# Performance work log

Hardware: AMD Instinct MI355X
Metric: run time of the kernel (lower is better)

Reference implementation:

```python
import jax, jax.numpy as jnp
import numpy as np
from jax import lax

N, DEG, D_IN, D_FEAT, D_HID, D_REP, G = 32768, 16, 128, 256, 256, 128, 64


def setup_inputs() -> dict:
    key = jax.random.key(0)
    ks = jax.random.split(key, 24)
    def w(k, shape):
        return (jax.random.normal(k, shape, jnp.float32) / np.sqrt(shape[0])).astype(jnp.float32)
    inp = {
        "in_feat": jax.random.normal(ks[0], (N, D_IN), jnp.float32),
        "neighbors": jax.random.randint(ks[1], (N, DEG), 0, N, jnp.int32),
        "node2graph": jnp.sort(jax.random.randint(ks[2], (N,), 0, G, jnp.int32)),
        # layer 1 (SAGEConv 128 -> 256, lstm aggregator: LSTM(128,128))
        "w_ih1": w(ks[3], (4 * D_IN, D_IN)),
        "w_hh1": w(ks[4], (4 * D_IN, D_IN)),
        "b_lstm1": jnp.zeros((4 * D_IN,), jnp.float32),
        "w_self1": w(ks[5], (D_IN, D_FEAT)),
        "w_neigh1": w(ks[6], (D_IN, D_FEAT)),
        "b1": jnp.zeros((D_FEAT,), jnp.float32),
        # layer 2 (SAGEConv 256 -> 256, LSTM(256,256))
        "w_ih2": w(ks[7], (4 * D_FEAT, D_FEAT)),
        "w_hh2": w(ks[8], (4 * D_FEAT, D_FEAT)),
        "b_lstm2": jnp.zeros((4 * D_FEAT,), jnp.float32),
        "w_self2": w(ks[9], (D_FEAT, D_HID)),
        "w_neigh2": w(ks[10], (D_FEAT, D_HID)),
        "b2": jnp.zeros((D_HID,), jnp.float32),
        # heads
        "w_mu": w(ks[11], (D_HID, D_REP)),
        "b_mu": jnp.zeros((D_REP,), jnp.float32),
        "w_sigma": w(ks[12], (D_HID, D_REP)),
        "b_sigma": jnp.zeros((D_REP,), jnp.float32),
    }
    return inp


def _lstm_agg(seq, w_ih, w_hh, b):
    # seq: [N, L, D] neighbor messages; LSTM with zero init, return final hidden h.
    n, _, d = seq.shape
    h0 = jnp.zeros((n, d), seq.dtype)
    def step(carry, x):
        h, c = carry
        gates = x @ w_ih.T + h @ w_hh.T + b  # [N, 4D]
        i, f, g, o = jnp.split(gates, 4, axis=-1)  # pytorch gate order i,f,g,o
        c = jax.nn.sigmoid(f) * c + jax.nn.sigmoid(i) * jnp.tanh(g)
        h = jax.nn.sigmoid(o) * jnp.tanh(c)
        return (h, c), None
    (h, _), _ = lax.scan(step, (h0, h0), jnp.swapaxes(seq, 0, 1))
    return h


def _sage_lstm(feat, neighbors, w_ih, w_hh, b_lstm, w_self, w_neigh, b):
    msgs = feat[neighbors]                      # irregular gather [N, DEG, D]
    h_n = _lstm_agg(msgs, w_ih, w_hh, b_lstm)   # [N, D]
    return feat @ w_self + h_n @ w_neigh + b


def reference(in_feat, neighbors, node2graph,
              w_ih1, w_hh1, b_lstm1, w_self1, w_neigh1, b1,
              w_ih2, w_hh2, b_lstm2, w_self2, w_neigh2, b2,
              w_mu, b_mu, w_sigma, b_sigma):
    h = _sage_lstm(in_feat, neighbors, w_ih1, w_hh1, b_lstm1, w_self1, w_neigh1, b1)
    h = jax.nn.relu(h)
    h = _sage_lstm(h, neighbors, w_ih2, w_hh2, b_lstm2, w_self2, w_neigh2, b2)
    # dgl.mean_nodes: per-graph mean over nodes
    sums = jax.ops.segment_sum(h, node2graph, num_segments=G)
    cnts = jax.ops.segment_sum(jnp.ones((h.shape[0],), h.dtype), node2graph, num_segments=G)
    x = sums / jnp.maximum(cnts, 1.0)[:, None]
    return (x @ w_mu + b_mu, x @ w_sigma + b_sigma)
```

## Files before the change

### kernel.cpp

```cpp
#include <hip/hip_runtime.h>
#include <hip/hip_bf16.h>
#include <cstddef>

#define NN_   32768
#define DEG_  16
#define D1_   128
#define D2_   256
#define G_    64
#define DREP_ 128

typedef __attribute__((ext_vector_type(8))) short bf16x8;
typedef __attribute__((ext_vector_type(4))) float f32x4;
typedef __attribute__((ext_vector_type(4))) unsigned short us4;
typedef unsigned short ushort_t;

__device__ __attribute__((aligned(16))) ushort_t g_feat1[(size_t)NN_ * D1_];
__device__ __attribute__((aligned(16))) ushort_t g_hfeat[(size_t)NN_ * D2_];
__device__ __attribute__((aligned(16))) ushort_t g_hA[(size_t)NN_ * D2_];
__device__ __attribute__((aligned(16))) ushort_t g_hB[(size_t)NN_ * D2_];
__device__ __attribute__((aligned(16))) ushort_t g_c[(size_t)NN_ * D2_];
__device__ __attribute__((aligned(16))) ushort_t g_P[(size_t)NN_ * 1024];
__device__ __attribute__((aligned(16))) float    g_outh[(size_t)NN_ * D2_];
__device__ __attribute__((aligned(16))) ushort_t g_wih1[512 * 128];
__device__ __attribute__((aligned(16))) ushort_t g_whh1[512 * 128];
__device__ __attribute__((aligned(16))) ushort_t g_wself1[256 * 128];
__device__ __attribute__((aligned(16))) ushort_t g_wneigh1[256 * 128];
__device__ __attribute__((aligned(16))) ushort_t g_wih2[1024 * 256];
__device__ __attribute__((aligned(16))) ushort_t g_whh2[1024 * 256];
__device__ __attribute__((aligned(16))) ushort_t g_wself2[256 * 256];
__device__ __attribute__((aligned(16))) ushort_t g_wneigh2[256 * 256];
__device__ float g_gsum[G_ * D2_];
__device__ int   g_gcnt[G_];

__device__ __forceinline__ ushort_t f2bf(float f) {
    unsigned int u = __float_as_uint(f);
    u += 0x7fffu + ((u >> 16) & 1u);
    return (ushort_t)(u >> 16);
}
__device__ __forceinline__ float bf2f(ushort_t u) {
    return __uint_as_float(((unsigned int)u) << 16);
}
__device__ __forceinline__ float sigf(float x) { return 1.f / (1.f + __expf(-x)); }
__device__ __forceinline__ float tanhf_(float x) { return 1.f - 2.f / (__expf(2.f * x) + 1.f); }

__global__ __launch_bounds__(256) void cvt_bf16(const float* __restrict__ src,
                                                ushort_t* __restrict__ dst, int n)
{
    int i = blockIdx.x * 256 + threadIdx.x;
    if (i < n) dst[i] = f2bf(src[i]);
}

__global__ __launch_bounds__(256) void cvt_bf16_T(const float* __restrict__ src,
                                                  ushort_t* __restrict__ dst, int K, int N)
{
    int i = blockIdx.x * 256 + threadIdx.x;
    if (i < K * N) {
        int k = i / N, n = i % N;
        dst[n * K + k] = f2bf(src[i]);
    }
}

template<bool DUAL, bool HAS_BIAS, bool RELU, bool OUTBF>
__global__ __launch_bounds__(256) void gemm_mfma(
    const ushort_t* __restrict__ A1, const ushort_t* __restrict__ B1,
    const ushort_t* __restrict__ A2, const ushort_t* __restrict__ B2,
    const float* __restrict__ bias, float* __restrict__ Cf,
    ushort_t* __restrict__ Cb, int M, int N, int K)
{
    __shared__ ushort_t As[64][72];
    __shared__ ushort_t Bs[64][72];
    const int tid = threadIdx.x;
    const int l = tid & 63, w = tid >> 6;
    const int m0 = blockIdx.y * 64, n0 = blockIdx.x * 64;

    f32x4 acc[4];
#pragma unroll
    for (int m = 0; m < 4; ++m) acc[m] = (f32x4){0.f, 0.f, 0.f, 0.f};

    const int npass = DUAL ? 2 : 1;
    for (int pass = 0; pass < npass; ++pass) {
        const ushort_t* __restrict__ A = (DUAL && pass) ? A2 : A1;
        const ushort_t* __restrict__ B = (DUAL && pass) ? B2 : B1;
        for (int k0 = 0; k0 < K; k0 += 64) {
#pragma unroll
            for (int i = 0; i < 2; ++i) {
                int cid = tid + 256 * i;
                int row = cid >> 3, col = (cid & 7) * 8;
                *(uint4*)&As[row][col] = *(const uint4*)&A[(size_t)(m0 + row) * K + k0 + col];
                *(uint4*)&Bs[row][col] = *(const uint4*)&B[(size_t)(n0 + row) * K + k0 + col];
            }
            __syncthreads();
#pragma unroll
            for (int kk = 0; kk < 64; kk += 32) {
                bf16x8 b = *(const bf16x8*)&Bs[16 * w + (l & 15)][kk + (l >> 4) * 8];
#pragma unroll
                for (int m = 0; m < 4; ++m) {
                    bf16x8 a = *(const bf16x8*)&As[16 * m + (l & 15)][kk + (l >> 4) * 8];
                    acc[m] = __builtin_amdgcn_mfma_f32_16x16x32_bf16(a, b, acc[m], 0, 0, 0);
                }
            }
            __syncthreads();
        }
    }

#pragma unroll
    for (int m = 0; m < 4; ++m) {
#pragma unroll
        for (int r = 0; r < 4; ++r) {
            int row = m0 + 16 * m + (l >> 4) * 4 + r;
            int col = n0 + 16 * w + (l & 15);
            float v = acc[m][r];
            if (HAS_BIAS) v += bias[col];
            if (RELU) v = fmaxf(v, 0.f);
            if (OUTBF) Cb[(size_t)row * N + col] = f2bf(v);
            else       Cf[(size_t)row * N + col] = v;
        }
    }
}

template<int D>
__global__ __launch_bounds__(256, 3) void lstm_step5(
    const ushort_t* __restrict__ h_prev, const ushort_t* __restrict__ whh,
    const ushort_t* __restrict__ P, const int* __restrict__ nbr,
    ushort_t* __restrict__ c, ushort_t* __restrict__ h_next, int t)
{
    constexpr int HP = D + 8;
    constexpr int KC = D / 32;
    constexpr int NT = 4;
    constexpr int NU = D / 64;
    __shared__ ushort_t As[64][HP];

    const int tid = threadIdx.x;
    const int l = tid & 63, w = tid >> 6;
    const int lr = l & 15, lg = l >> 4;
    const int m0 = blockIdx.x * 64;

    int js[NT];
#pragma unroll
    for (int nt = 0; nt < NT; ++nt)
        js[nt] = nbr[(size_t)(m0 + nt * 16 + lr) * DEG_ + t];

    constexpr int CH = 64 * D / 8;
#pragma unroll
    for (int cid = tid; cid < CH; cid += 256) {
        int row = cid / (D / 8), cc = (cid % (D / 8)) * 8;
        *(uint4*)&As[row][cc] = *(const uint4*)&h_prev[(size_t)(m0 + row) * D + cc];
    }
    __syncthreads();

#pragma unroll
    for (int u = 0; u < NU; ++u) {
        const int d0 = u * 64;
        const int dd = d0 + w * 16 + lg * 4;

        us4 pg[NT][4];
#pragma unroll
        for (int nt = 0; nt < NT; ++nt) {
            const size_t base = (size_t)js[nt] * (4 * D) + dd;
#pragma unroll
            for (int g = 0; g < 4; ++g)
                pg[nt][g] = *(const us4*)&P[base + g * D];
        }

        f32x4 acc[4][NT];
#pragma unroll
        for (int g = 0; g < 4; ++g)
#pragma unroll
            for (int nt = 0; nt < NT; ++nt) acc[g][nt] = (f32x4){0.f, 0.f, 0.f, 0.f};

        const ushort_t* __restrict__ wbase =
            &whh[(size_t)(d0 + w * 16 + lr) * D + lg * 8];
#pragma unroll
        for (int kc = 0; kc < KC; ++kc) {
            bf16x8 a[4];
#pragma unroll
            for (int g = 0; g < 4; ++g)
                a[g] = *(const bf16x8*)&wbase[(size_t)g * D * D + kc * 32];
#pragma unroll
            for (int nt = 0; nt < NT; ++nt) {
                bf16x8 b = *(const bf16x8*)&As[nt * 16 + lr][kc * 32 + lg * 8];
#pragma unroll
                for (int g = 0; g < 4; ++g)
                    acc[g][nt] = __builtin_amdgcn_mfma_f32_16x16x32_bf16(
                        a[g], b, acc[g][nt], 0, 0, 0);
            }
        }

#pragma unroll
        for (int nt = 0; nt < NT; ++nt) {
            const size_t ci = (size_t)(m0 + nt * 16 + lr) * D + dd;
            us4 cold = *(const us4*)&c[ci];
            us4 cnew, hnew;
#pragma unroll
            for (int r = 0; r < 4; ++r) {
                float gi = acc[0][nt][r] + bf2f(pg[nt][0][r]);
                float gf = acc[1][nt][r] + bf2f(pg[nt][1][r]);
                float gg = acc[2][nt][r] + bf2f(pg[nt][2][r]);
                float go = acc[3][nt][r] + bf2f(pg[nt][3][r]);
                float cn = sigf(gf) * bf2f(cold[r]) + sigf(gi) * tanhf_(gg);
                cnew[r] = f2bf(cn);
                hnew[r] = f2bf(sigf(go) * tanhf_(cn));
            }
            *(us4*)&c[ci] = cnew;
            *(us4*)&h_next[ci] = hnew;
        }
    }
}

template<int D>
__global__ __launch_bounds__(256) void cell_first(
    const ushort_t* __restrict__ P, const int* __restrict__ nbr,
    ushort_t* __restrict__ c, ushort_t* __restrict__ h_out)
{
    int idx = blockIdx.x * 256 + threadIdx.x;
    int n = idx / D, d = idx % D;
    int j = nbr[n * DEG_];
    size_t base = (size_t)j * (4 * D);
    float gi = bf2f(P[base + d]);
    float gg = bf2f(P[base + 2 * D + d]);
    float go = bf2f(P[base + 3 * D + d]);
    float cn = sigf(gi) * tanhf_(gg);
    c[idx] = f2bf(cn);
    h_out[idx] = f2bf(sigf(go) * tanhf_(cn));
}

__global__ void graph_counts(const int* __restrict__ n2g, int* __restrict__ cnt)
{
    __shared__ int lb[G_ + 1];
    int g = threadIdx.x;
    if (g <= G_) {
        int lo = 0, hi = NN_;
        while (lo < hi) {
            int mid = (lo + hi) >> 1;
            if (n2g[mid] < g) lo = mid + 1; else hi = mid;
        }
        lb[g] = lo;
    }
    __syncthreads();
    if (g < G_) cnt[g] = lb[g + 1] - lb[g];
}

__global__ __launch_bounds__(256) void seg_sum(
    const float* __restrict__ X, const int* __restrict__ n2g,
    float* __restrict__ gsum)
{
    int d = threadIdx.x;
    int n_start = blockIdx.x * 64;
    int cur = n2g[n_start];
    float acc = 0.f;
    for (int n = n_start; n < n_start + 64; ++n) {
        int g = n2g[n];
        if (g != cur) {
            atomicAdd(&gsum[cur * D2_ + d], acc);
            acc = 0.f;
            cur = g;
        }
        acc += X[(size_t)n * D2_ + d];
    }
    atomicAdd(&gsum[cur * D2_ + d], acc);
}

__global__ __launch_bounds__(128) void head_kernel(
    const float* __restrict__ gsum, const int* __restrict__ cnt,
    const float* __restrict__ w_mu, const float* __restrict__ b_mu,
    const float* __restrict__ w_sig, const float* __restrict__ b_sig,
    float* __restrict__ out)
{
    __shared__ float x[D2_];
    int g = blockIdx.x, j = threadIdx.x;
    float inv = 1.f / fmaxf((float)cnt[g], 1.f);
    x[j] = gsum[g * D2_ + j] * inv;
    x[j + 128] = gsum[g * D2_ + 128 + j] * inv;
    __syncthreads();
    float mu = b_mu[j], sg = b_sig[j];
    for (int k = 0; k < D2_; ++k) {
        float xv = x[k];
        mu += xv * w_mu[k * DREP_ + j];
        sg += xv * w_sig[k * DREP_ + j];
    }
    out[g * DREP_ + j] = mu;
    out[G_ * DREP_ + g * DREP_ + j] = sg;
}

extern "C" void kernel_launch(void* const* d_in, const int* in_sizes, int n_in,
                              void* d_out, int out_size, void* d_ws, size_t ws_size,
                              hipStream_t stream)
{
    const float* in_feat   = (const float*)d_in[0];
    const int*   neighbors = (const int*)d_in[1];
    const int*   node2graph= (const int*)d_in[2];
    const float* w_ih1     = (const float*)d_in[3];
    const float* w_hh1     = (const float*)d_in[4];
    const float* b_lstm1   = (const float*)d_in[5];
    const float* w_self1   = (const float*)d_in[6];
    const float* w_neigh1  = (const float*)d_in[7];
    const float* b1        = (const float*)d_in[8];
    const float* w_ih2     = (const float*)d_in[9];
    const float* w_hh2     = (const float*)d_in[10];
    const float* b_lstm2   = (const float*)d_in[11];
    const float* w_self2   = (const float*)d_in[12];
    const float* w_neigh2  = (const float*)d_in[13];
    const float* b2        = (const float*)d_in[14];
    const float* w_mu      = (const float*)d_in[15];
    const float* b_mu      = (const float*)d_in[16];
    const float* w_sigma   = (const float*)d_in[17];
    const float* b_sigma   = (const float*)d_in[18];

    void *pF1, *pHF, *pHA, *pHB, *pC, *pP, *pOH;
    void *pWI1, *pWH1, *pWS1, *pWN1, *pWI2, *pWH2, *pWS2, *pWN2, *pGS, *pGC;
    hipGetSymbolAddress(&pF1, HIP_SYMBOL(g_feat1));
    hipGetSymbolAddress(&pHF, HIP_SYMBOL(g_hfeat));
    hipGetSymbolAddress(&pHA, HIP_SYMBOL(g_hA));
    hipGetSymbolAddress(&pHB, HIP_SYMBOL(g_hB));
    hipGetSymbolAddress(&pC,  HIP_SYMBOL(g_c));
    hipGetSymbolAddress(&pP,  HIP_SYMBOL(g_P));
    hipGetSymbolAddress(&pOH, HIP_SYMBOL(g_outh));
    hipGetSymbolAddress(&pWI1, HIP_SYMBOL(g_wih1));
    hipGetSymbolAddress(&pWH1, HIP_SYMBOL(g_whh1));
    hipGetSymbolAddress(&pWS1, HIP_SYMBOL(g_wself1));
    hipGetSymbolAddress(&pWN1, HIP_SYMBOL(g_wneigh1));
    hipGetSymbolAddress(&pWI2, HIP_SYMBOL(g_wih2));
    hipGetSymbolAddress(&pWH2, HIP_SYMBOL(g_whh2));
    hipGetSymbolAddress(&pWS2, HIP_SYMBOL(g_wself2));
    hipGetSymbolAddress(&pWN2, HIP_SYMBOL(g_wneigh2));
    hipGetSymbolAddress(&pGS, HIP_SYMBOL(g_gsum));
    hipGetSymbolAddress(&pGC, HIP_SYMBOL(g_gcnt));

    ushort_t* feat1 = (ushort_t*)pF1;
    ushort_t* hfeat = (ushort_t*)pHF;
    ushort_t* hA    = (ushort_t*)pHA;
    ushort_t* hB    = (ushort_t*)pHB;
    ushort_t* c     = (ushort_t*)pC;
    ushort_t* P     = (ushort_t*)pP;
    float*    outh  = (float*)pOH;
    ushort_t* wih1  = (ushort_t*)pWI1;
    ushort_t* whh1  = (ushort_t*)pWH1;
    ushort_t* wself1= (ushort_t*)pWS1;
    ushort_t* wneigh1=(ushort_t*)pWN1;
    ushort_t* wih2  = (ushort_t*)pWI2;
    ushort_t* whh2  = (ushort_t*)pWH2;
    ushort_t* wself2= (ushort_t*)pWS2;
    ushort_t* wneigh2=(ushort_t*)pWN2;
    float*    gsum  = (float*)pGS;
    int*      gcnt  = (int*)pGC;

    cvt_bf16<<<(NN_ * D1_ + 255) / 256, 256, 0, stream>>>(in_feat, feat1, NN_ * D1_);
    cvt_bf16<<<(512 * 128 + 255) / 256, 256, 0, stream>>>(w_ih1, wih1, 512 * 128);
    cvt_bf16<<<(512 * 128 + 255) / 256, 256, 0, stream>>>(w_hh1, whh1, 512 * 128);
    cvt_bf16_T<<<(128 * 256 + 255) / 256, 256, 0, stream>>>(w_self1, wself1, 128, 256);
    cvt_bf16_T<<<(128 * 256 + 255) / 256, 256, 0, stream>>>(w_neigh1, wneigh1, 128, 256);
    cvt_bf16<<<(1024 * 256 + 255) / 256, 256, 0, stream>>>(w_ih2, wih2, 1024 * 256);
    cvt_bf16<<<(1024 * 256 + 255) / 256, 256, 0, stream>>>(w_hh2, whh2, 1024 * 256);
    cvt_bf16_T<<<(256 * 256 + 255) / 256, 256, 0, stream>>>(w_self2, wself2, 256, 256);
    cvt_bf16_T<<<(256 * 256 + 255) / 256, 256, 0, stream>>>(w_neigh2, wneigh2, 256, 256);

    gemm_mfma<false, true, false, true>
        <<<dim3(512 / 64, NN_ / 64), 256, 0, stream>>>(
            feat1, wih1, nullptr, nullptr, b_lstm1, nullptr, P, NN_, 512, D1_);

    cell_first<D1_><<<(NN_ * D1_) / 256, 256, 0, stream>>>(P, neighbors, c, hA);
    for (int t = 1; t < DEG_; ++t) {
        const ushort_t* hp = (t & 1) ? hA : hB;
        ushort_t*       hn = (t & 1) ? hB : hA;
        lstm_step5<D1_><<<NN_ / 64, 256, 0, stream>>>(
            hp, whh1, P, neighbors, c, hn, t);
    }

    gemm_mfma<true, true, true, true>
        <<<dim3(256 / 64, NN_ / 64), 256, 0, stream>>>(
            feat1, wself1, hB, wneigh1, b1, nullptr, hfeat, NN_, D2_, D1_);

    gemm_mfma<false, true, false, true>
        <<<dim3(1024 / 64, NN_ / 64), 256, 0, stream>>>(
            hfeat, wih2, nullptr, nullptr, b_lstm2, nullptr, P, NN_, 1024, D2_);

    cell_first<D2_><<<(NN_ * D2_) / 256, 256, 0, stream>>>(P, neighbors, c, hA);
    for (int t = 1; t < DEG_; ++t) {
        const ushort_t* hp = (t & 1) ? hA : hB;
        ushort_t*       hn = (t & 1) ? hB : hA;
        lstm_step5<D2_><<<NN_ / 64, 256, 0, stream>>>(
            hp, whh2, P, neighbors, c, hn, t);
    }

    gemm_mfma<true, true, false, false>
        <<<dim3(256 / 64, NN_ / 64), 256, 0, stream>>>(
            hfeat, wself2, hB, wneigh2, b2, outh, nullptr, NN_, D2_, D2_);

    hipMemsetAsync(gsum, 0, (size_t)G_ * D2_ * sizeof(float), stream);
    graph_counts<<<1, 128, 0, stream>>>(node2graph, gcnt);
    seg_sum<<<NN_ / 64, 256, 0, stream>>>(outh, node2graph, gsum);
    head_kernel<<<G_, 128, 0, stream>>>(gsum, gcnt, w_mu, b_mu, w_sigma, b_sigma,
                                        (float*)d_out);
}
```

Measured before the change: 1.605 ms.

## Fuse input projection into LSTM step kernels, dropping precomputed gate buffer

Removes the per-node precomputed input-projection buffer P and its GEMM, and instead each LSTM step gathers raw neighbor features into shared memory and computes W_ih·x alongside W_hh·h with MFMA. The first step becomes a specialized variant of the same kernel. This cuts the gathered bytes per step by 4x and removes a large intermediate write, but recomputes the input projection for every step (16x more input-projection FLOPs) and lowers occupancy due to doubled shared memory and reduced launch bounds.

```diff
diff --git a/kernel.cpp b/kernel.cpp
--- a/kernel.cpp
+++ b/kernel.cpp
@@ -19,7 +19,6 @@
 __device__ __attribute__((aligned(16))) ushort_t g_hA[(size_t)NN_ * D2_];
 __device__ __attribute__((aligned(16))) ushort_t g_hB[(size_t)NN_ * D2_];
 __device__ __attribute__((aligned(16))) ushort_t g_c[(size_t)NN_ * D2_];
-__device__ __attribute__((aligned(16))) ushort_t g_P[(size_t)NN_ * 1024];
 __device__ __attribute__((aligned(16))) float    g_outh[(size_t)NN_ * D2_];
 __device__ __attribute__((aligned(16))) ushort_t g_wih1[512 * 128];
 __device__ __attribute__((aligned(16))) ushort_t g_whh1[512 * 128];
@@ -118,33 +117,36 @@
     }
 }
 
-template<int D>
-__global__ __launch_bounds__(256, 3) void lstm_step5(
-    const ushort_t* __restrict__ h_prev, const ushort_t* __restrict__ whh,
-    const ushort_t* __restrict__ P, const int* __restrict__ nbr,
+template<int D, bool FIRST>
+__global__ __launch_bounds__(256, 2) void lstm_fused(
+    const ushort_t* __restrict__ feats,
+    const ushort_t* __restrict__ wih,
+    const ushort_t* __restrict__ whh,
+    const ushort_t* __restrict__ h_prev,
+    const int* __restrict__ nbr,
+    const float* __restrict__ b_lstm,
     ushort_t* __restrict__ c, ushort_t* __restrict__ h_next, int t)
 {
     constexpr int HP = D + 8;
     constexpr int KC = D / 32;
     constexpr int NT = 4;
     constexpr int NU = D / 64;
-    __shared__ ushort_t As[64][HP];
+    __shared__ ushort_t Ms[64][HP];
+    __shared__ ushort_t Hs[64][HP];
 
     const int tid = threadIdx.x;
     const int l = tid & 63, w = tid >> 6;
     const int lr = l & 15, lg = l >> 4;
-    const int m0 = blockIdx.x * 64;
-
-    int js[NT];
-#pragma unroll
-    for (int nt = 0; nt < NT; ++nt)
-        js[nt] = nbr[(size_t)(m0 + nt * 16 + lr) * DEG_ + t];
+    const int n0 = blockIdx.x * 64;
 
     constexpr int CH = 64 * D / 8;
 #pragma unroll
     for (int cid = tid; cid < CH; cid += 256) {
         int row = cid / (D / 8), cc = (cid % (D / 8)) * 8;
-        *(uint4*)&As[row][cc] = *(const uint4*)&h_prev[(size_t)(m0 + row) * D + cc];
+        int j = nbr[(size_t)(n0 + row) * DEG_ + t];
+        *(uint4*)&Ms[row][cc] = *(const uint4*)&feats[(size_t)j * D + cc];
+        if (!FIRST)
+            *(uint4*)&Hs[row][cc] = *(const uint4*)&h_prev[(size_t)(n0 + row) * D + cc];
     }
     __syncthreads();
 
@@ -152,52 +154,66 @@
     for (int u = 0; u < NU; ++u) {
         const int d0 = u * 64;
         const int dd = d0 + w * 16 + lg * 4;
-
-        us4 pg[NT][4];
-#pragma unroll
-        for (int nt = 0; nt < NT; ++nt) {
-            const size_t base = (size_t)js[nt] * (4 * D) + dd;
+        const int drow = d0 + w * 16 + lr;
+
+        f32x4 acc[4][NT];
+#pragma unroll
+        for (int g = 0; g < 4; ++g)
+#pragma unroll
+            for (int nt = 0; nt < NT; ++nt) acc[g][nt] = (f32x4){0.f, 0.f, 0.f, 0.f};
+
+        const ushort_t* __restrict__ wib = &wih[(size_t)drow * D + lg * 8];
+        const ushort_t* __restrict__ whb = &whh[(size_t)drow * D + lg * 8];
+
+#pragma unroll
+        for (int kc = 0; kc < KC; ++kc) {
+            bf16x8 ai[4];
 #pragma unroll
             for (int g = 0; g < 4; ++g)
-                pg[nt][g] = *(const us4*)&P[base + g * D];
-        }
-
-        f32x4 acc[4][NT];
-#pragma unroll
-        for (int g = 0; g < 4; ++g)
-#pragma unroll
-            for (int nt = 0; nt < NT; ++nt) acc[g][nt] = (f32x4){0.f, 0.f, 0.f, 0.f};
-
-        const ushort_t* __restrict__ wbase =
-            &whh[(size_t)(d0 + w * 16 + lr) * D + lg * 8];
-#pragma unroll
-        for (int kc = 0; kc < KC; ++kc) {
-            bf16x8 a[4];
-#pragma unroll
-            for (int g = 0; g < 4; ++g)
-                a[g] = *(const bf16x8*)&wbase[(size_t)g * D * D + kc * 32];
+                ai[g] = *(const bf16x8*)&wib[(size_t)g * D * D + kc * 32];
 #pragma unroll
             for (int nt = 0; nt < NT; ++nt) {
-                bf16x8 b = *(const bf16x8*)&As[nt * 16 + lr][kc * 32 + lg * 8];
+                bf16x8 bm = *(const bf16x8*)&Ms[nt * 16 + lr][kc * 32 + lg * 8];
 #pragma unroll
                 for (int g = 0; g < 4; ++g)
                     acc[g][nt] = __builtin_amdgcn_mfma_f32_16x16x32_bf16(
-                        a[g], b, acc[g][nt], 0, 0, 0);
-            }
-        }
+                        ai[g], bm, acc[g][nt], 0, 0, 0);
+            }
+            if (!FIRST) {
+                bf16x8 ah[4];
+#pragma unroll
+                for (int g = 0; g < 4; ++g)
+                    ah[g] = *(const bf16x8*)&whb[(size_t)g * D * D + kc * 32];
+#pragma unroll
+                for (int nt = 0; nt < NT; ++nt) {
+                    bf16x8 bh = *(const bf16x8*)&Hs[nt * 16 + lr][kc * 32 + lg * 8];
+#pragma unroll
+                    for (int g = 0; g < 4; ++g)
+                        acc[g][nt] = __builtin_amdgcn_mfma_f32_16x16x32_bf16(
+                            ah[g], bh, acc[g][nt], 0, 0, 0);
+                }
+            }
+        }
+
+        f32x4 bi[4];
+#pragma unroll
+        for (int g = 0; g < 4; ++g)
+            bi[g] = *(const f32x4*)&b_lstm[g * D + dd];
 
 #pragma unroll
         for (int nt = 0; nt < NT; ++nt) {
-            const size_t ci = (size_t)(m0 + nt * 16 + lr) * D + dd;
-            us4 cold = *(const us4*)&c[ci];
+            const size_t ci = (size_t)(n0 + nt * 16 + lr) * D + dd;
+            us4 cold = (us4){0, 0, 0, 0};
+            if (!FIRST) cold = *(const us4*)&c[ci];
             us4 cnew, hnew;
 #pragma unroll
             for (int r = 0; r < 4; ++r) {
-                float gi = acc[0][nt][r] + bf2f(pg[nt][0][r]);
-                float gf = acc[1][nt][r] + bf2f(pg[nt][1][r]);
-                float gg = acc[2][nt][r] + bf2f(pg[nt][2][r]);
-                float go = acc[3][nt][r] + bf2f(pg[nt][3][r]);
-                float cn = sigf(gf) * bf2f(cold[r]) + sigf(gi) * tanhf_(gg);
+                float gi = acc[0][nt][r] + bi[0][r];
+                float gf = acc[1][nt][r] + bi[1][r];
+                float gg = acc[2][nt][r] + bi[2][r];
+                float go = acc[3][nt][r] + bi[3][r];
+                float cp = FIRST ? 0.f : bf2f(cold[r]);
+                float cn = sigf(gf) * cp + sigf(gi) * tanhf_(gg);
                 cnew[r] = f2bf(cn);
                 hnew[r] = f2bf(sigf(go) * tanhf_(cn));
             }
@@ -205,23 +221,6 @@
             *(us4*)&h_next[ci] = hnew;
         }
     }
-}
-
-template<int D>
-__global__ __launch_bounds__(256) void cell_first(
-    const ushort_t* __restrict__ P, const int* __restrict__ nbr,
-    ushort_t* __restrict__ c, ushort_t* __restrict__ h_out)
-{
-    int idx = blockIdx.x * 256 + threadIdx.x;
-    int n = idx / D, d = idx % D;
-    int j = nbr[n * DEG_];
-    size_t base = (size_t)j * (4 * D);
-    float gi = bf2f(P[base + d]);
-    float gg = bf2f(P[base + 2 * D + d]);
-    float go = bf2f(P[base + 3 * D + d]);
-    float cn = sigf(gi) * tanhf_(gg);
-    c[idx] = f2bf(cn);
-    h_out[idx] = f2bf(sigf(go) * tanhf_(cn));
 }
 
 __global__ void graph_counts(const int* __restrict__ n2g, int* __restrict__ cnt)
@@ -306,14 +305,13 @@
     const float* w_sigma   = (const float*)d_in[17];
     const float* b_sigma   = (const float*)d_in[18];
 
-    void *pF1, *pHF, *pHA, *pHB, *pC, *pP, *pOH;
+    void *pF1, *pHF, *pHA, *pHB, *pC, *pOH;
     void *pWI1, *pWH1, *pWS1, *pWN1, *pWI2, *pWH2, *pWS2, *pWN2, *pGS, *pGC;
     hipGetSymbolAddress(&pF1, HIP_SYMBOL(g_feat1));
     hipGetSymbolAddress(&pHF, HIP_SYMBOL(g_hfeat));
     hipGetSymbolAddress(&pHA, HIP_SYMBOL(g_hA));
     hipGetSymbolAddress(&pHB, HIP_SYMBOL(g_hB));
     hipGetSymbolAddress(&pC,  HIP_SYMBOL(g_c));
-    hipGetSymbolAddress(&pP,  HIP_SYMBOL(g_P));
     hipGetSymbolAddress(&pOH, HIP_SYMBOL(g_outh));
     hipGetSymbolAddress(&pWI1, HIP_SYMBOL(g_wih1));
     hipGetSymbolAddress(&pWH1, HIP_SYMBOL(g_whh1));
@@ -331,7 +329,6 @@
     ushort_t* hA    = (ushort_t*)pHA;
     ushort_t* hB    = (ushort_t*)pHB;
     ushort_t* c     = (ushort_t*)pC;
-    ushort_t* P     = (ushort_t*)pP;
     float*    outh  = (float*)pOH;
     ushort_t* wih1  = (ushort_t*)pWI1;
     ushort_t* whh1  = (ushort_t*)pWH1;
@@ -354,32 +351,30 @@
     cvt_bf16_T<<<(256 * 256 + 255) / 256, 256, 0, stream>>>(w_self2, wself2, 256, 256);
     cvt_bf16_T<<<(256 * 256 + 255) / 256, 256, 0, stream>>>(w_neigh2, wneigh2, 256, 256);
 
-    gemm_mfma<false, true, false, true>
-        <<<dim3(512 / 64, NN_ / 64), 256, 0, stream>>>(
-            feat1, wih1, nullptr, nullptr, b_lstm1, nullptr, P, NN_, 512, D1_);
-
-    cell_first<D1_><<<(NN_ * D1_) / 256, 256, 0, stream>>>(P, neighbors, c, hA);
-    for (int t = 1; t < DEG_; ++t) {
+    for (int t = 0; t < DEG_; ++t) {
         const ushort_t* hp = (t & 1) ? hA : hB;
         ushort_t*       hn = (t & 1) ? hB : hA;
-        lstm_step5<D1_><<<NN_ / 64, 256, 0, stream>>>(
-            hp, whh1, P, neighbors, c, hn, t);
+        if (t == 0)
+            lstm_fused<D1_, true><<<NN_ / 64, 256, 0, stream>>>(
+                feat1, wih1, whh1, hp, neighbors, b_lstm1, c, hn, 0);
+        else
+            lstm_fused<D1_, false><<<NN_ / 64, 256, 0, stream>>>(
+                feat1, wih1, whh1, hp, neighbors, b_lstm1, c, hn, t);
     }
 
     gemm_mfma<true, true, true, true>
         <<<dim3(256 / 64, NN_ / 64), 256, 0, stream>>>(
             feat1, wself1, hB, wneigh1, b1, nullptr, hfeat, NN_, D2_, D1_);
 
-    gemm_mfma<false, true, false, true>
-        <<<dim3(1024 / 64, NN_ / 64), 256, 0, stream>>>(
-            hfeat, wih2, nullptr, nullptr, b_lstm2, nullptr, P, NN_, 1024, D2_);
-
-    cell_first<D2_><<<(NN_ * D2_) / 256, 256, 0, stream>>>(P, neighbors, c, hA);
-    for (int t = 1; t < DEG_; ++t) {
+    for (int t = 0; t < DEG_; ++t) {
         const ushort_t* hp = (t & 1) ? hA : hB;
         ushort_t*       hn = (t & 1) ? hB : hA;
-        lstm_step5<D2_><<<NN_ / 64, 256, 0, stream>>>(
-            hp, whh2, P, neighbors, c, hn, t);
+        if (t == 0)
+            lstm_fused<D2_, true><<<NN_ / 64, 256, 0, stream>>>(
+                hfeat, wih2, whh2, hp, neighbors, b_lstm2, c, hn, 0);
+        else
+            lstm_fused<D2_, false><<<NN_ / 64, 256, 0, stream>>>(
+                hfeat, wih2, whh2, hp, neighbors, b_lstm2, c, hn, t);
     }
 
     gemm_mfma<true, true, false, false>
```

Result: slower. 2.730 ms (+70.1%).
